# Kernel tuning notes

Measured on AMD Instinct MI355X. Metric: run time of the kernel, lower is better.

The kernel has to match this reference:

```python
import jax, jax.numpy as jnp
import numpy as np

N = 40000      # nodes
E = 640000     # edges (avg degree 16)
F = 128        # in_feats
OUT = 128      # out_feats


def setup_inputs() -> dict:
    key = jax.random.key(0)
    ks = jax.random.split(key, 8)
    feat = jax.random.normal(ks[0], (N, F), dtype=jnp.float32)
    src = jax.random.randint(ks[1], (E,), 0, N, dtype=jnp.int32)
    dst = jnp.sort(jax.random.randint(ks[2], (E,), 0, N, dtype=jnp.int32))
    # AttentionAGG: fc1 (2F -> F), fc2 (F -> 1); fc_layer (2F -> OUT)
    s1 = 1.0 / np.sqrt(2 * F)
    s2 = 1.0 / np.sqrt(F)
    w1 = jax.random.normal(ks[3], (2 * F, F), dtype=jnp.float32) * s1
    b1 = jnp.zeros((F,), dtype=jnp.float32)
    w2 = jax.random.normal(ks[4], (F, 1), dtype=jnp.float32) * s2
    b2 = jnp.zeros((1,), dtype=jnp.float32)
    wf = jax.random.normal(ks[5], (2 * F, OUT), dtype=jnp.float32) * s1
    bf = jnp.zeros((OUT,), dtype=jnp.float32)
    return {"feat": feat, "src": src, "dst": dst,
            "w1": w1, "b1": b1, "w2": w2, "b2": b2, "wf": wf, "bf": bf}


def reference(feat, src, dst, w1, b1, w2, b2, wf, bf):
    f = feat.shape[1]
    n = feat.shape[0]
    # fc1(concat(h_dst, m_src)) == h_dst @ w1[:F] + h_src @ w1[F:]  (edge_weight is None)
    proj_dst = feat @ w1[:f]          # [N, F]
    proj_src = feat @ w1[f:]          # [N, F]
    pre = jnp.tanh(proj_dst[dst] + proj_src[src] + b1)   # [E, F]
    scores = (pre @ w2)[:, 0] + b2[0]                    # [E]
    # softmax over the ragged incoming-edge set of each dst node
    smax = jax.ops.segment_max(scores, dst, num_segments=n, indices_are_sorted=True)
    ex = jnp.exp(scores - jax.lax.stop_gradient(smax)[dst])
    den = jax.ops.segment_sum(ex, dst, num_segments=n, indices_are_sorted=True)
    att = ex / den[dst]                                  # [E]
    # weighted segment-sum of messages (m_e = feat[src]); zero-degree nodes get 0
    neigh = jax.ops.segment_sum(att[:, None] * feat[src], dst,
                                num_segments=n, indices_are_sorted=True)  # [N, F]
    # fc_layer(concat(h_self, neigh))
    rst = feat @ wf[:f] + neigh @ wf[f:] + bf            # [N, OUT]
    return rst
```

## Files before the change

kernel.cpp:

```cpp
#include <hip/hip_runtime.h>
#include <math.h>

#define F 128
#define OUT 128

typedef unsigned short ushort_t;
typedef __attribute__((ext_vector_type(8))) short bfrag;
typedef __attribute__((ext_vector_type(4))) float ffrag;
typedef __attribute__((ext_vector_type(2))) float fx2;

__device__ __forceinline__ float bf_lo(unsigned int u) {
    return __uint_as_float(u << 16);
}
__device__ __forceinline__ float bf_hi(unsigned int u) {
    return __uint_as_float(u & 0xffff0000u);
}
__device__ __forceinline__ ushort_t f2bf(float f) {
    unsigned int x = __float_as_uint(f);
    unsigned int r = x + 0x7fffu + ((x >> 16) & 1u);
    return (ushort_t)(r >> 16);
}
__device__ __forceinline__ unsigned pk2(float lo, float hi) {
    return (unsigned)f2bf(lo) | ((unsigned)f2bf(hi) << 16);
}

#define DPP_ADD(x, ctrl) \
    ((x) + __int_as_float(__builtin_amdgcn_update_dpp( \
        0, __float_as_int(x), (ctrl), 0xf, 0xf, true)))


__global__ __launch_bounds__(256) void tiny_prep_kernel(
    const float* __restrict__ w1, const float* __restrict__ wf,
    const int* __restrict__ dst, ushort_t* __restrict__ btp,
    ushort_t* __restrict__ btf, int* __restrict__ row_ptr,
    int n, int e, int nb1, int nb2)
{
    const int b = blockIdx.x, t = threadIdx.x;
    if (b < nb1) {
        int idx = b * 256 + t;
        int j = idx >> 7, k = idx & 127;
        float v = (j < F) ? w1[(size_t)k * F + j]
                          : w1[(size_t)(F + k) * F + (j - F)];
        btp[idx] = f2bf(v);
    } else if (b < nb1 + nb2) {
        int idx = (b - nb1) * 256 + t;
        int j = idx >> 8, k = idx & 255;
        btf[idx] = f2bf(wf[(size_t)k * F + j]);
    } else {
        int i = (b - nb1 - nb2) * 256 + t;
        if (i >= e) return;
        int d = dst[i];
        int prev = (i == 0) ? -1 : dst[i - 1];
        for (int v = prev + 1; v <= d; ++v) row_ptr[v] = i;
        if (i == e - 1) {
            for (int v = d + 1; v <= n; ++v) row_ptr[v] = e;
        }
    }
}

#define PST 136
__global__ __launch_bounds__(256) void proj_gemm_kernel(
    const float* __restrict__ feat, const ushort_t* __restrict__ btp,
    const float* __restrict__ b1, ushort_t* __restrict__ abig,
    ushort_t* __restrict__ e_dst, ushort_t* __restrict__ srcpack, int n)
{
    __shared__ ushort_t As[64 * PST];
    __shared__ ushort_t Ep[4][16 * 80];
    const int t = threadIdx.x;
    const int wv = t >> 6, lane = t & 63;
    const int lm = lane & 15, quad = lane >> 4;
    const int row0 = blockIdx.x * 64, col0 = wv * 64;

#pragma unroll
    for (int k = 0; k < 4; ++k) {
        int l = k * 256 + t;
        int r = l >> 4, c = (l & 15) * 8;
        int grow = row0 + r;
        float4 a = make_float4(0.f, 0.f, 0.f, 0.f);
        float4 bb = make_float4(0.f, 0.f, 0.f, 0.f);
        if (grow < n) {
            a = *(const float4*)(feat + (size_t)grow * F + c);
            bb = *(const float4*)(feat + (size_t)grow * F + c + 4);
        }
        unsigned p0 = pk2(a.x, a.y), p1 = pk2(a.z, a.w);
        unsigned p2 = pk2(bb.x, bb.y), p3 = pk2(bb.z, bb.w);
        *(uint4*)(As + r * PST + c) = make_uint4(p0, p1, p2, p3);
        if (grow < n) {
            *(uint4*)(abig + (size_t)grow * 256 + c) = make_uint4(p0, p1, p2, p3);
            unsigned w01 = (unsigned)__builtin_amdgcn_cvt_pk_fp8_f32(a.x, a.y, 0, false);
            w01 = (unsigned)__builtin_amdgcn_cvt_pk_fp8_f32(a.z, a.w, (int)w01, true);
            unsigned w23 = (unsigned)__builtin_amdgcn_cvt_pk_fp8_f32(bb.x, bb.y, 0, false);
            w23 = (unsigned)__builtin_amdgcn_cvt_pk_fp8_f32(bb.z, bb.w, (int)w23, true);
            char* rb = (char*)srcpack + (size_t)grow * 256;
            *(unsigned*)(rb + c * 2 + 4) = w01;
            *(unsigned*)(rb + c * 2 + 12) = w23;
        }
    }
    __syncthreads();

    bfrag bfr[4][4];
#pragma unroll
    for (int ks = 0; ks < 4; ++ks)
#pragma unroll
        for (int ni = 0; ni < 4; ++ni)
            bfr[ks][ni] = *(const bfrag*)(btp + (size_t)(col0 + ni * 16 + lm) * 128
                                          + ks * 32 + quad * 8);

    ffrag acc[4][4];
#pragma unroll
    for (int mi = 0; mi < 4; ++mi)
#pragma unroll
        for (int ni = 0; ni < 4; ++ni) acc[mi][ni] = (ffrag){0.f, 0.f, 0.f, 0.f};

#pragma unroll
    for (int ks = 0; ks < 4; ++ks)
#pragma unroll
        for (int mi = 0; mi < 4; ++mi) {
            bfrag af = *(const bfrag*)(As + (mi * 16 + lm) * PST + ks * 32 + quad * 8);
#pragma unroll
            for (int ni = 0; ni < 4; ++ni)
                acc[mi][ni] = __builtin_amdgcn_mfma_f32_16x16x32_bf16(
                    af, bfr[ks][ni], acc[mi][ni], 0, 0, 0);
        }

    float bias[4];
#pragma unroll
    for (int ni = 0; ni < 4; ++ni)
        bias[ni] = (col0 < F) ? b1[col0 + ni * 16 + lm] : 0.f;

#pragma unroll
    for (int mi = 0; mi < 4; ++mi) {
#pragma unroll
        for (int ni = 0; ni < 4; ++ni)
#pragma unroll
            for (int r = 0; r < 4; ++r)
                Ep[wv][(quad * 4 + r) * 80 + ni * 16 + lm] =
                    f2bf(__expf(2.f * (acc[mi][ni][r] + bias[ni])));
#pragma unroll
        for (int ps = 0; ps < 2; ++ps) {
            int rl = ps * 8 + (lane >> 3), co = (lane & 7) * 8;
            uint4 vv = *(const uint4*)(&Ep[wv][rl * 80 + co]);
            int grow = row0 + mi * 16 + rl;
            if (grow < n) {
                if (col0 < F) {
                    *(uint4*)(e_dst + (size_t)grow * F + col0 + co) = vv;
                } else {
                    int f0 = col0 - F + co;
                    unsigned b0 = (unsigned)__builtin_amdgcn_cvt_pk_bf8_f32(
                        bf_lo(vv.x), bf_hi(vv.x), 0, false);
                    b0 = (unsigned)__builtin_amdgcn_cvt_pk_bf8_f32(
                        bf_lo(vv.y), bf_hi(vv.y), (int)b0, true);
                    unsigned b1v = (unsigned)__builtin_amdgcn_cvt_pk_bf8_f32(
                        bf_lo(vv.z), bf_hi(vv.z), 0, false);
                    b1v = (unsigned)__builtin_amdgcn_cvt_pk_bf8_f32(
                        bf_lo(vv.w), bf_hi(vv.w), (int)b1v, true);
                    char* rb = (char*)srcpack + (size_t)grow * 256;
                    *(unsigned*)(rb + f0 * 2) = b0;
                    *(unsigned*)(rb + f0 * 2 + 8) = b1v;
                }
            }
        }
    }
}

__global__ __launch_bounds__(256) void fused_kernel(
    const ushort_t* __restrict__ e_dst, const ushort_t* __restrict__ srcpack,
    const int* __restrict__ src, const int* __restrict__ row_ptr,
    const float* __restrict__ w2, ushort_t* __restrict__ abig, int n)
{
    const int v = (int)((blockIdx.x * 256u + threadIdx.x) >> 5);
    const int fl = threadIdx.x & 31;
    const int sbase = threadIdx.x & 32;

    const float4 wv4 = ((const float4*)w2)[fl];
    const float w0 = wv4.x, w1_ = wv4.y, w2_ = wv4.z, w3_ = wv4.w;
    float sw = w0 + w1_ + w2_ + w3_;
    float aw = fabsf(w0) + fabsf(w1_) + fabsf(w2_) + fabsf(w3_);
#pragma unroll
    for (int off = 16; off; off >>= 1) {
        sw += __shfl_xor(sw, off, 64);
        aw += __shfl_xor(aw, off, 64);
    }
    const float K = sw - aw;
    const float L2E = 1.4426950408889634f;
    const float K2 = K * L2E;

    if (v >= n) return;
    const int begin = row_ptr[v], end = row_ptr[v + 1];

    const uint2 ud = *(const uint2*)(e_dst + (size_t)v * F + fl * 4);
    const float ea0 = bf_lo(ud.x), ea1 = bf_hi(ud.x);
    const float ea2 = bf_lo(ud.y), ea3 = bf_hi(ud.y);

    const uint2* __restrict__ sp = (const uint2*)srcpack + fl;

    float s = 0.f, a0 = 0.f, a1 = 0.f, a2 = 0.f, a3 = 0.f;

    for (int cb = begin; cb < end; cb += 32) {
        const int clen = min(32, end - cb);
        const int sv = (fl < clen) ? src[cb + fl] : 0;
        int jj = 0;
        for (; jj + 4 <= clen; jj += 4) {
            uint2 u[4];
#pragma unroll
            for (int q = 0; q < 4; ++q) {
                const int sq = __shfl(sv, sbase + jj + q, 64);
                u[q] = sp[(size_t)sq * 32];
            }
            float p[4];
#pragma unroll
            for (int q = 0; q < 4; ++q) {
                fx2 eslo = __builtin_amdgcn_cvt_pk_f32_bf8((int)u[q].x, false);
                fx2 eshi = __builtin_amdgcn_cvt_pk_f32_bf8((int)u[q].x, true);
                float A = fmaf(ea0, eslo[0], 1.f);
                float B = fmaf(ea1, eslo[1], 1.f);
                float C = fmaf(ea2, eshi[0], 1.f);
                float D = fmaf(ea3, eshi[1], 1.f);
                float nAB = fmaf(w0, B, w1_ * A);
                float nCD = fmaf(w2_, D, w3_ * C);
                float rAB = __builtin_amdgcn_rcpf(A * B);
                float rCD = __builtin_amdgcn_rcpf(C * D);
                p[q] = fmaf(nAB, rAB, nCD * rCD);
            }
#pragma unroll
            for (int q = 0; q < 4; ++q) {
                p[q] = DPP_ADD(p[q], 0x121);
                p[q] = DPP_ADD(p[q], 0x122);
                p[q] = DPP_ADD(p[q], 0x124);
                p[q] = DPP_ADD(p[q], 0x128);
                p[q] += __shfl_xor(p[q], 16, 64);
            }
            float g[4];
#pragma unroll
            for (int q = 0; q < 4; ++q)
                g[q] = exp2f(fmaf(-2.f * L2E, p[q], K2));
            s += (g[0] + g[1]) + (g[2] + g[3]);
#pragma unroll
            for (int q = 0; q < 4; ++q) {
                fx2 lo = __builtin_amdgcn_cvt_pk_f32_fp8((int)u[q].y, false);
                fx2 hi = __builtin_amdgcn_cvt_pk_f32_fp8((int)u[q].y, true);
                a0 = fmaf(g[q], lo[0], a0);
                a1 = fmaf(g[q], lo[1], a1);
                a2 = fmaf(g[q], hi[0], a2);
                a3 = fmaf(g[q], hi[1], a3);
            }
        }
        for (; jj < clen; ++jj) {
            const int s0 = __shfl(sv, sbase + jj, 64);
            const uint2 u0 = sp[(size_t)s0 * 32];
            fx2 eslo = __builtin_amdgcn_cvt_pk_f32_bf8((int)u0.x, false);
            fx2 eshi = __builtin_amdgcn_cvt_pk_f32_bf8((int)u0.x, true);
            float A = fmaf(ea0, eslo[0], 1.f);
            float B = fmaf(ea1, eslo[1], 1.f);
            float C = fmaf(ea2, eshi[0], 1.f);
            float D = fmaf(ea3, eshi[1], 1.f);
            float nAB = fmaf(w0, B, w1_ * A);
            float nCD = fmaf(w2_, D, w3_ * C);
            float rAB = __builtin_amdgcn_rcpf(A * B);
            float rCD = __builtin_amdgcn_rcpf(C * D);
            float p0 = fmaf(nAB, rAB, nCD * rCD);
            p0 = DPP_ADD(p0, 0x121);
            p0 = DPP_ADD(p0, 0x122);
            p0 = DPP_ADD(p0, 0x124);
            p0 = DPP_ADD(p0, 0x128);
            p0 += __shfl_xor(p0, 16, 64);
            const float g0 = exp2f(fmaf(-2.f * L2E, p0, K2));
            s += g0;
            fx2 lo = __builtin_amdgcn_cvt_pk_f32_fp8((int)u0.y, false);
            fx2 hi = __builtin_amdgcn_cvt_pk_f32_fp8((int)u0.y, true);
            a0 = fmaf(g0, lo[0], a0);
            a1 = fmaf(g0, lo[1], a1);
            a2 = fmaf(g0, hi[0], a2);
            a3 = fmaf(g0, hi[1], a3);
        }
    }

    const float inv = (end > begin) ? 1.f / s : 0.f;
    ushort4 o = make_ushort4(f2bf(a0 * inv), f2bf(a1 * inv),
                             f2bf(a2 * inv), f2bf(a3 * inv));
    *(ushort4*)(abig + (size_t)v * 256 + 128 + fl * 4) = o;
}

#define OST 280
#define EFS 36
__global__ __launch_bounds__(256) void out_gemm_kernel(
    const ushort_t* __restrict__ abig, const ushort_t* __restrict__ btf,
    const float* __restrict__ bfv, float* __restrict__ out, int n)
{
    __shared__ ushort_t As[64 * OST];
    __shared__ float Ef[4][16 * EFS];
    const int t = threadIdx.x;
    const int wv = t >> 6, lane = t & 63;
    const int lm = lane & 15, quad = lane >> 4;
    const int row0 = blockIdx.x * 64, col0 = wv * 32;

#pragma unroll
    for (int k = 0; k < 8; ++k) {
        int l = k * 256 + t;
        int r = l >> 5, ch = l & 31;
        uint4 d = make_uint4(0, 0, 0, 0);
        if (row0 + r < n) d = *(const uint4*)(abig + (size_t)(row0 + r) * 256 + ch * 8);
        *(uint4*)(As + r * OST + ch * 8) = d;
    }
    __syncthreads();

    bfrag bfr[8][2];
#pragma unroll
    for (int ks = 0; ks < 8; ++ks)
#pragma unroll
        for (int ni = 0; ni < 2; ++ni)
            bfr[ks][ni] = *(const bfrag*)(btf + (size_t)(col0 + ni * 16 + lm) * 256
                                          + ks * 32 + quad * 8);

    ffrag acc[4][2];
#pragma unroll
    for (int mi = 0; mi < 4; ++mi)
#pragma unroll
        for (int ni = 0; ni < 2; ++ni) acc[mi][ni] = (ffrag){0.f, 0.f, 0.f, 0.f};

#pragma unroll
    for (int ks = 0; ks < 8; ++ks)
#pragma unroll
        for (int mi = 0; mi < 4; ++mi) {
            bfrag af = *(const bfrag*)(As + (mi * 16 + lm) * OST + ks * 32 + quad * 8);
#pragma unroll
            for (int ni = 0; ni < 2; ++ni)
                acc[mi][ni] = __builtin_amdgcn_mfma_f32_16x16x32_bf16(
                    af, bfr[ks][ni], acc[mi][ni], 0, 0, 0);
        }

    float bb[2];
#pragma unroll
    for (int ni = 0; ni < 2; ++ni) bb[ni] = bfv[col0 + ni * 16 + lm];

#pragma unroll
    for (int mi = 0; mi < 4; ++mi) {
#pragma unroll
        for (int ni = 0; ni < 2; ++ni)
#pragma unroll
            for (int r = 0; r < 4; ++r)
                Ef[wv][(quad * 4 + r) * EFS + ni * 16 + lm] = acc[mi][ni][r] + bb[ni];
#pragma unroll
        for (int ps = 0; ps < 2; ++ps) {
            int rl = ps * 8 + (lane >> 3), co = (lane & 7) * 4;
            float4 vv = *(const float4*)(&Ef[wv][rl * EFS + co]);
            int grow = row0 + mi * 16 + rl;
            if (grow < n)
                *(float4*)(out + (size_t)grow * OUT + col0 + co) = vv;
        }
    }
}

extern "C" void kernel_launch(void* const* d_in, const int* in_sizes, int n_in,
                              void* d_out, int out_size, void* d_ws, size_t ws_size,
                              hipStream_t stream)
{
    const float* feat = (const float*)d_in[0];
    const int*   src  = (const int*)d_in[1];
    const int*   dst  = (const int*)d_in[2];
    const float* w1   = (const float*)d_in[3];
    const float* b1   = (const float*)d_in[4];
    const float* w2   = (const float*)d_in[5];
    const float* b2   = (const float*)d_in[6];  (void)b2;
    const float* wf   = (const float*)d_in[7];
    const float* bfv  = (const float*)d_in[8];
    float* out = (float*)d_out;

    const int n = in_sizes[0] / F;
    const int e = in_sizes[1];

    ushort_t* abig    = (ushort_t*)d_ws;
    ushort_t* e_dst   = abig + (size_t)n * 256;
    ushort_t* srcpack = e_dst + (size_t)n * 128;
    ushort_t* btp     = srcpack + (size_t)n * 128;
    ushort_t* btf     = btp + 32768;
    int* row_ptr      = (int*)(btf + 32768);

    const int nb1 = 128, nb2 = 128;
    const int nb3 = (e + 255) / 256;

    tiny_prep_kernel<<<nb1 + nb2 + nb3, 256, 0, stream>>>(
        w1, wf, dst, btp, btf, row_ptr, n, e, nb1, nb2);
    proj_gemm_kernel<<<(n + 63) / 64, 256, 0, stream>>>(
        feat, btp, b1, abig, e_dst, srcpack, n);
    fused_kernel<<<(n + 7) / 8, 256, 0, stream>>>(
        e_dst, srcpack, src, row_ptr, w2, abig, n);
    out_gemm_kernel<<<(n + 63) / 64, 256, 0, stream>>>(abig, btf, bfv, out, n);
}
```

Baseline: 149.9 us.

## Process four edges per wavefront in parallel with 16 lanes per edge

Result: no change. 150.7 us (median of 2 runs) (+0.5%).

```diff
diff --git a/kernel.cpp b/kernel.cpp
--- a/kernel.cpp
+++ b/kernel.cpp
@@ -168,117 +168,88 @@
     const int* __restrict__ src, const int* __restrict__ row_ptr,
     const float* __restrict__ w2, ushort_t* __restrict__ abig, int n)
 {
-    const int v = (int)((blockIdx.x * 256u + threadIdx.x) >> 5);
-    const int fl = threadIdx.x & 31;
-    const int sbase = threadIdx.x & 32;
-
-    const float4 wv4 = ((const float4*)w2)[fl];
-    const float w0 = wv4.x, w1_ = wv4.y, w2_ = wv4.z, w3_ = wv4.w;
-    float sw = w0 + w1_ + w2_ + w3_;
-    float aw = fabsf(w0) + fabsf(w1_) + fabsf(w2_) + fabsf(w3_);
-#pragma unroll
-    for (int off = 16; off; off >>= 1) {
+    const int v = (int)(blockIdx.x * 4u + (threadIdx.x >> 6));
+    const int flane = threadIdx.x & 15;
+    const int row = (threadIdx.x >> 4) & 3;
+
+    const float4 wa = ((const float4*)w2)[2 * flane];
+    const float4 wb = ((const float4*)w2)[2 * flane + 1];
+    float sw = (wa.x + wa.y + wa.z + wa.w) + (wb.x + wb.y + wb.z + wb.w);
+    float aw = fabsf(wa.x) + fabsf(wa.y) + fabsf(wa.z) + fabsf(wa.w)
+             + fabsf(wb.x) + fabsf(wb.y) + fabsf(wb.z) + fabsf(wb.w);
+#pragma unroll
+    for (int off = 8; off; off >>= 1) {
         sw += __shfl_xor(sw, off, 64);
         aw += __shfl_xor(aw, off, 64);
     }
-    const float K = sw - aw;
     const float L2E = 1.4426950408889634f;
-    const float K2 = K * L2E;
+    const float K2 = (sw - aw) * L2E;
 
     if (v >= n) return;
     const int begin = row_ptr[v], end = row_ptr[v + 1];
 
-    const uint2 ud = *(const uint2*)(e_dst + (size_t)v * F + fl * 4);
+    const uint4 ud = *(const uint4*)(e_dst + (size_t)v * F + flane * 8);
     const float ea0 = bf_lo(ud.x), ea1 = bf_hi(ud.x);
     const float ea2 = bf_lo(ud.y), ea3 = bf_hi(ud.y);
-
-    const uint2* __restrict__ sp = (const uint2*)srcpack + fl;
-
-    float s = 0.f, a0 = 0.f, a1 = 0.f, a2 = 0.f, a3 = 0.f;
-
-    for (int cb = begin; cb < end; cb += 32) {
-        const int clen = min(32, end - cb);
-        const int sv = (fl < clen) ? src[cb + fl] : 0;
-        int jj = 0;
-        for (; jj + 4 <= clen; jj += 4) {
-            uint2 u[4];
-#pragma unroll
-            for (int q = 0; q < 4; ++q) {
-                const int sq = __shfl(sv, sbase + jj + q, 64);
-                u[q] = sp[(size_t)sq * 32];
-            }
-            float p[4];
-#pragma unroll
-            for (int q = 0; q < 4; ++q) {
-                fx2 eslo = __builtin_amdgcn_cvt_pk_f32_bf8((int)u[q].x, false);
-                fx2 eshi = __builtin_amdgcn_cvt_pk_f32_bf8((int)u[q].x, true);
-                float A = fmaf(ea0, eslo[0], 1.f);
-                float B = fmaf(ea1, eslo[1], 1.f);
-                float C = fmaf(ea2, eshi[0], 1.f);
-                float D = fmaf(ea3, eshi[1], 1.f);
-                float nAB = fmaf(w0, B, w1_ * A);
-                float nCD = fmaf(w2_, D, w3_ * C);
-                float rAB = __builtin_amdgcn_rcpf(A * B);
-                float rCD = __builtin_amdgcn_rcpf(C * D);
-                p[q] = fmaf(nAB, rAB, nCD * rCD);
-            }
-#pragma unroll
-            for (int q = 0; q < 4; ++q) {
-                p[q] = DPP_ADD(p[q], 0x121);
-                p[q] = DPP_ADD(p[q], 0x122);
-                p[q] = DPP_ADD(p[q], 0x124);
-                p[q] = DPP_ADD(p[q], 0x128);
-                p[q] += __shfl_xor(p[q], 16, 64);
-            }
-            float g[4];
-#pragma unroll
-            for (int q = 0; q < 4; ++q)
-                g[q] = exp2f(fmaf(-2.f * L2E, p[q], K2));
-            s += (g[0] + g[1]) + (g[2] + g[3]);
-#pragma unroll
-            for (int q = 0; q < 4; ++q) {
-                fx2 lo = __builtin_amdgcn_cvt_pk_f32_fp8((int)u[q].y, false);
-                fx2 hi = __builtin_amdgcn_cvt_pk_f32_fp8((int)u[q].y, true);
-                a0 = fmaf(g[q], lo[0], a0);
-                a1 = fmaf(g[q], lo[1], a1);
-                a2 = fmaf(g[q], hi[0], a2);
-                a3 = fmaf(g[q], hi[1], a3);
-            }
-        }
-        for (; jj < clen; ++jj) {
-            const int s0 = __shfl(sv, sbase + jj, 64);
-            const uint2 u0 = sp[(size_t)s0 * 32];
-            fx2 eslo = __builtin_amdgcn_cvt_pk_f32_bf8((int)u0.x, false);
-            fx2 eshi = __builtin_amdgcn_cvt_pk_f32_bf8((int)u0.x, true);
-            float A = fmaf(ea0, eslo[0], 1.f);
-            float B = fmaf(ea1, eslo[1], 1.f);
-            float C = fmaf(ea2, eshi[0], 1.f);
-            float D = fmaf(ea3, eshi[1], 1.f);
-            float nAB = fmaf(w0, B, w1_ * A);
-            float nCD = fmaf(w2_, D, w3_ * C);
-            float rAB = __builtin_amdgcn_rcpf(A * B);
-            float rCD = __builtin_amdgcn_rcpf(C * D);
-            float p0 = fmaf(nAB, rAB, nCD * rCD);
-            p0 = DPP_ADD(p0, 0x121);
-            p0 = DPP_ADD(p0, 0x122);
-            p0 = DPP_ADD(p0, 0x124);
-            p0 = DPP_ADD(p0, 0x128);
-            p0 += __shfl_xor(p0, 16, 64);
-            const float g0 = exp2f(fmaf(-2.f * L2E, p0, K2));
-            s += g0;
-            fx2 lo = __builtin_amdgcn_cvt_pk_f32_fp8((int)u0.y, false);
-            fx2 hi = __builtin_amdgcn_cvt_pk_f32_fp8((int)u0.y, true);
-            a0 = fmaf(g0, lo[0], a0);
-            a1 = fmaf(g0, lo[1], a1);
-            a2 = fmaf(g0, hi[0], a2);
-            a3 = fmaf(g0, hi[1], a3);
-        }
-    }
+    const float ea4 = bf_lo(ud.z), ea5 = bf_hi(ud.z);
+    const float ea6 = bf_lo(ud.w), ea7 = bf_hi(ud.w);
+
+    const uint4* __restrict__ sp = (const uint4*)srcpack;
+
+    float s = 0.f;
+    float a0 = 0.f, a1 = 0.f, a2 = 0.f, a3 = 0.f;
+    float a4 = 0.f, a5 = 0.f, a6 = 0.f, a7 = 0.f;
+
+    for (int cb = begin; cb < end; cb += 4) {
+        const int ed = cb + row;
+        const bool valid = ed < end;
+        const int sq = src[valid ? ed : end - 1];
+        const uint4 u = sp[(size_t)sq * 16 + flane];
+        fx2 e01 = __builtin_amdgcn_cvt_pk_f32_bf8((int)u.x, false);
+        fx2 e23 = __builtin_amdgcn_cvt_pk_f32_bf8((int)u.x, true);
+        fx2 e45 = __builtin_amdgcn_cvt_pk_f32_bf8((int)u.z, false);
+        fx2 e67 = __builtin_amdgcn_cvt_pk_f32_bf8((int)u.z, true);
+        float A = fmaf(ea0, e01[0], 1.f), B = fmaf(ea1, e01[1], 1.f);
+        float C = fmaf(ea2, e23[0], 1.f), D = fmaf(ea3, e23[1], 1.f);
+        float E = fmaf(ea4, e45[0], 1.f), G = fmaf(ea5, e45[1], 1.f);
+        float H = fmaf(ea6, e67[0], 1.f), I = fmaf(ea7, e67[1], 1.f);
+        float p;
+        p = fmaf(wa.x, B, wa.y * A) * __builtin_amdgcn_rcpf(A * B);
+        p = fmaf(fmaf(wa.z, D, wa.w * C), __builtin_amdgcn_rcpf(C * D), p);
+        p = fmaf(fmaf(wb.x, G, wb.y * E), __builtin_amdgcn_rcpf(E * G), p);
+        p = fmaf(fmaf(wb.z, I, wb.w * H), __builtin_amdgcn_rcpf(H * I), p);
+        p = DPP_ADD(p, 0x121);
+        p = DPP_ADD(p, 0x122);
+        p = DPP_ADD(p, 0x124);
+        p = DPP_ADD(p, 0x128);
+        const float g = valid ? exp2f(fmaf(-2.f * L2E, p, K2)) : 0.f;
+        s += g;
+        fx2 f01 = __builtin_amdgcn_cvt_pk_f32_fp8((int)u.y, false);
+        fx2 f23 = __builtin_amdgcn_cvt_pk_f32_fp8((int)u.y, true);
+        fx2 f45 = __builtin_amdgcn_cvt_pk_f32_fp8((int)u.w, false);
+        fx2 f67 = __builtin_amdgcn_cvt_pk_f32_fp8((int)u.w, true);
+        a0 = fmaf(g, f01[0], a0); a1 = fmaf(g, f01[1], a1);
+        a2 = fmaf(g, f23[0], a2); a3 = fmaf(g, f23[1], a3);
+        a4 = fmaf(g, f45[0], a4); a5 = fmaf(g, f45[1], a5);
+        a6 = fmaf(g, f67[0], a6); a7 = fmaf(g, f67[1], a7);
+    }
+
+    s += __shfl_xor(s, 16, 64);  s += __shfl_xor(s, 32, 64);
+    a0 += __shfl_xor(a0, 16, 64); a0 += __shfl_xor(a0, 32, 64);
+    a1 += __shfl_xor(a1, 16, 64); a1 += __shfl_xor(a1, 32, 64);
+    a2 += __shfl_xor(a2, 16, 64); a2 += __shfl_xor(a2, 32, 64);
+    a3 += __shfl_xor(a3, 16, 64); a3 += __shfl_xor(a3, 32, 64);
+    a4 += __shfl_xor(a4, 16, 64); a4 += __shfl_xor(a4, 32, 64);
+    a5 += __shfl_xor(a5, 16, 64); a5 += __shfl_xor(a5, 32, 64);
+    a6 += __shfl_xor(a6, 16, 64); a6 += __shfl_xor(a6, 32, 64);
+    a7 += __shfl_xor(a7, 16, 64); a7 += __shfl_xor(a7, 32, 64);
 
     const float inv = (end > begin) ? 1.f / s : 0.f;
-    ushort4 o = make_ushort4(f2bf(a0 * inv), f2bf(a1 * inv),
-                             f2bf(a2 * inv), f2bf(a3 * inv));
-    *(ushort4*)(abig + (size_t)v * 256 + 128 + fl * 4) = o;
+    if (row == 0) {
+        uint4 o = make_uint4(pk2(a0 * inv, a1 * inv), pk2(a2 * inv, a3 * inv),
+                             pk2(a4 * inv, a5 * inv), pk2(a6 * inv, a7 * inv));
+        *(uint4*)(abig + (size_t)v * 256 + 128 + flane * 8) = o;
+    }
 }
 
 #define OST 280
@@ -383,7 +354,7 @@
         w1, wf, dst, btp, btf, row_ptr, n, e, nb1, nb2);
     proj_gemm_kernel<<<(n + 63) / 64, 256, 0, stream>>>(
         feat, btp, b1, abig, e_dst, srcpack, n);
-    fused_kernel<<<(n + 7) / 8, 256, 0, stream>>>(
+    fused_kernel<<<(n + 3) / 4, 256, 0, stream>>>(
         e_dst, srcpack, src, row_ptr, w2, abig, n);
     out_gemm_kernel<<<(n + 63) / 64, 256, 0, stream>>>(abig, btf, bfv, out, n);
 }
```
